# Performance work log

Measured on AMD Instinct MI355X. Metric: run time of the kernel, lower is better.

## Reference

```python
import jax, jax.numpy as jnp
import numpy as np

E = 64      # n_routed_experts
T = 32768   # total routed tokens
K = 1024    # hidden_size
I = 512     # moe_intermediate_size
C = 1024


def setup_inputs() -> dict:
    key = jax.random.key(0)
    k1, k2, k3 = jax.random.split(key, 3)
    x = jax.random.normal(k1, (T, K), dtype=jnp.float32)
    # uniform routing: 512 tokens per expert, sums to T
    tokens_per_expert = jnp.full((E,), T // E, dtype=jnp.int32)
    w13 = jax.random.normal(k2, (E, K, 2 * I), dtype=jnp.float32) * 0.02  # fused w1/w3
    w2 = jax.random.normal(k3, (E, I, K), dtype=jnp.float32) * 0.02
    return {"x": x, "tokens_per_expert": tokens_per_expert, "w13": w13, "w2": w2, "decoding": 0}


def reference(x, tokens_per_expert, w13, w2, decoding):
    # Tokens are laid out contiguously by expert (grouped-GEMM convention).
    starts = jnp.cumsum(tokens_per_expert) - tokens_per_expert           # [E]
    eid = jnp.repeat(jnp.arange(E), tokens_per_expert, total_repeat_length=T)  # [T]
    pos = jnp.arange(T) - starts[eid]                                    # slot within expert
    # dispatch to dense [E, C, K] buffer (zero-padded beyond each expert's count)
    xb = jnp.zeros((E, C, K), x.dtype).at[eid, pos].set(x)
    # grouped GEMM 1: fused w1w3  -> [E, C, 2I]
    gate_up = jnp.einsum('eck,ekn->ecn', xb, w13)
    # SwiGLU: split last dim into gate / up
    gate, up = jnp.split(gate_up, 2, axis=-1)
    h = jax.nn.silu(gate) * up                                           # [E, C, I]
    # grouped GEMM 2: fused w2 -> [E, C, K]
    yb = jnp.einsum('eci,eik->eck', h, w2)
    # gather back to token order [T, K]
    return yb[eid, pos]
```

## Files before the change

### kernel.cpp

```cpp
#include <hip/hip_runtime.h>
#include <hip/hip_bf16.h>
#include <stdint.h>

#define NEXP 64
#define TTOK 32768
#define HID  1024
#define IMID 512
#define CAP  1024

typedef __bf16 bf16x8 __attribute__((ext_vector_type(8)));
typedef float  f32x4  __attribute__((ext_vector_type(4)));

static __device__ __forceinline__ unsigned int f2bf_u(float f) {
    __hip_bfloat16 h = __float2bfloat16(f);
    return (unsigned int)*reinterpret_cast<unsigned short*>(&h);
}
static __device__ __forceinline__ unsigned int pack2(float lo, float hi) {
    return f2bf_u(lo) | (f2bf_u(hi) << 16);
}
static __device__ __forceinline__ unsigned short f2bf_s(float f) {
    __hip_bfloat16 h = __float2bfloat16(f);
    return *reinterpret_cast<unsigned short*>(&h);
}

static __device__ __forceinline__ void gload16(const void* g, void* l) {
    __builtin_amdgcn_global_load_lds(
        (const __attribute__((address_space(1))) unsigned int*)g,
        (__attribute__((address_space(3))) unsigned int*)l,
        16, 0, 0);
}

static __device__ __forceinline__ int expert_start(const int* tpe, int e, int lane) {
    int v = tpe[lane];
    int contrib = (lane < e) ? v : 0;
    #pragma unroll
    for (int off = 1; off < 64; off <<= 1)
        contrib += __shfl_xor(contrib, off, 64);
    return contrib;
}

__global__ __launch_bounds__(256)
void cvt_all_k(const float* __restrict__ x, unsigned short* __restrict__ xbf,
               const float* __restrict__ w13, unsigned short* __restrict__ w13p) {
    const int bid = blockIdx.x;
    const int t   = threadIdx.x;

    if (bid < 16384) {
        const int n0 = (bid & 15) * 64;
        const int k0 = ((bid >> 4) & 15) * 64;
        const int e  = bid >> 8;
        __shared__ unsigned short Tl[64][72];
        const int kl = t >> 4, nl = (t & 15) * 4;
        const float* src = w13 + ((size_t)e << 20) + (size_t)k0 * 1024 + n0;
        #pragma unroll
        for (int p = 0; p < 4; ++p) {
            int k = kl + p * 16;
            f32x4 v = *reinterpret_cast<const f32x4*>(src + (size_t)k * 1024 + nl);
            uint2 wv; wv.x = pack2(v.x, v.y); wv.y = pack2(v.z, v.w);
            *reinterpret_cast<uint2*>(&Tl[k][nl]) = wv;
        }
        __syncthreads();
        const int nloc = t >> 2, kc = (t & 3) * 16;
        const int n = n0 + nloc;
        const int icol = n & 511, isup = n >> 9;
        const int np = (icol >> 5) * 64 + isup * 32 + (icol & 31);
        unsigned int v32[8];
        #pragma unroll
        for (int j = 0; j < 8; ++j)
            v32[j] = (unsigned int)Tl[kc + 2 * j][nloc] |
                     ((unsigned int)Tl[kc + 2 * j + 1][nloc] << 16);
        unsigned short* dst = w13p + ((size_t)e << 20) + (size_t)np * 1024 + k0 + kc;
        uint4 o0 = {v32[0], v32[1], v32[2], v32[3]};
        uint4 o1 = {v32[4], v32[5], v32[6], v32[7]};
        *reinterpret_cast<uint4*>(dst)     = o0;
        *reinterpret_cast<uint4*>(dst + 8) = o1;
    } else {
        size_t i = ((size_t)(bid - 16384) * 256 + t) * 8;
        f32x4 a = *reinterpret_cast<const f32x4*>(x + i);
        f32x4 b = *reinterpret_cast<const f32x4*>(x + i + 4);
        uint4 o;
        o.x = pack2(a.x, a.y); o.y = pack2(a.z, a.w);
        o.z = pack2(b.x, b.y); o.w = pack2(b.z, b.w);
        *reinterpret_cast<uint4*>(xbf + i) = o;
    }
}

static __device__ __forceinline__ void w2_tile_cvt(const float* __restrict__ w2,
                                                   unsigned short* __restrict__ w2p,
                                                   int tile, int t, char* lds) {
    const int e  = tile >> 7;
    const int k0 = ((tile >> 4) & 7) * 64;
    const int n0 = (tile & 15) * 64;
    unsigned short (*Tl)[72] = reinterpret_cast<unsigned short(*)[72]>(lds);
    const int kl = t >> 4, nl = (t & 15) * 4;
    const float* src = w2 + (size_t)e * (IMID * HID) + (size_t)k0 * 1024 + n0;
    #pragma unroll
    for (int p = 0; p < 4; ++p) {
        int k = kl + p * 16;
        f32x4 v = *reinterpret_cast<const f32x4*>(src + (size_t)k * 1024 + nl);
        uint2 wv; wv.x = pack2(v.x, v.y); wv.y = pack2(v.z, v.w);
        *reinterpret_cast<uint2*>(&Tl[k][nl]) = wv;
    }
    __syncthreads();
    const int nloc = t >> 2, kc = (t & 3) * 16;
    unsigned int v32[8];
    #pragma unroll
    for (int j = 0; j < 8; ++j)
        v32[j] = (unsigned int)Tl[kc + 2 * j][nloc] |
                 ((unsigned int)Tl[kc + 2 * j + 1][nloc] << 16);
    unsigned short* dst = w2p + (size_t)e * (HID * IMID) + (size_t)(n0 + nloc) * IMID + k0 + kc;
    uint4 o0 = {v32[0], v32[1], v32[2], v32[3]};
    uint4 o1 = {v32[4], v32[5], v32[6], v32[7]};
    *reinterpret_cast<uint4*>(dst)     = o0;
    *reinterpret_cast<uint4*>(dst + 8) = o1;
}

__global__ __launch_bounds__(256, 2)
void gemm1(const unsigned short* __restrict__ xbf,
           const int* __restrict__ tpe,
           const unsigned short* __restrict__ w13p,
           unsigned short* __restrict__ hbuf,
           const float* __restrict__ w2,
           unsigned short* __restrict__ w2p) {
    __shared__ alignas(16) char lds[49152];
    const int bid = blockIdx.x;
    const int t = threadIdx.x, lane = t & 63, w = t >> 6;

    if (bid >= 2048) {
        w2_tile_cvt(w2, w2p, bid - 2048, t, lds);
        return;
    }

    const int work = (bid & 7) * 256 + (bid >> 3);
    const int e  = work >> 5;
    const int nt = (work >> 3) & 3;
    const int mt = work & 7;

    int cnt = tpe[e]; if (cnt > CAP) cnt = CAP;
    const int m0 = mt * 128;
    if (m0 >= cnt) return;
    const int start = expert_start(tpe, e, lane);

    char* As = lds;
    char* Bs = lds + 16384;
    const int wr = w >> 1, wc = w & 1;
    const int r = lane & 15, q = lane >> 4;

    f32x4 acc[4][8];
    const f32x4 z4 = {0.f, 0.f, 0.f, 0.f};
    #pragma unroll
    for (int i = 0; i < 4; ++i)
        #pragma unroll
        for (int j = 0; j < 8; ++j) acc[i][j] = z4;

    const int swb = ((lane & 7) ^ (lane >> 3)) << 4;
    const char* aP = (const char*)xbf;
    const char* bP = (const char*)w13p + ((size_t)e << 21) + ((size_t)nt << 19);

    for (int kt = 0; kt < 16; ++kt) {
        __syncthreads();
        const int kb = kt * 128;
        #pragma unroll
        for (int i = 0; i < 4; ++i) {
            const int srow = w * 32 + i * 8 + (lane >> 3);
            long ar = (long)start + m0 + srow;
            if (ar > TTOK - 1) ar = TTOK - 1;
            gload16(aP + ar * 2048 + kb + swb, As + w * 4096 + i * 1024);
        }
        #pragma unroll
        for (int i = 0; i < 8; ++i) {
            const int srow = w * 64 + i * 8 + (lane >> 3);
            gload16(bP + (size_t)srow * 2048 + kb + swb, Bs + w * 8192 + i * 1024);
        }
        __syncthreads();
        #pragma unroll
        for (int kk = 0; kk < 2; ++kk) {
            bf16x8 af[4], bf[8];
            #pragma unroll
            for (int fm = 0; fm < 4; ++fm) {
                int row = (wr << 6) + (fm << 4) + r;
                af[fm] = *reinterpret_cast<const bf16x8*>(
                    As + row * 128 + ((kk * 64 + q * 16) ^ ((row & 7) << 4)));
            }
            #pragma unroll
            for (int fn = 0; fn < 8; ++fn) {
                int row = (wc << 7) + (fn << 4) + r;
                bf[fn] = *reinterpret_cast<const bf16x8*>(
                    Bs + row * 128 + ((kk * 64 + q * 16) ^ ((row & 7) << 4)));
            }
            #pragma unroll
            for (int fm = 0; fm < 4; ++fm)
                #pragma unroll
                for (int fn = 0; fn < 8; ++fn)
                    acc[fm][fn] = __builtin_amdgcn_mfma_f32_16x16x32_bf16(
                        af[fm], bf[fn], acc[fm][fn], 0, 0, 0);
        }
    }

    #pragma unroll
    for (int fm = 0; fm < 4; ++fm) {
        int mb = m0 + (wr << 6) + (fm << 4) + (q << 2);
        #pragma unroll
        for (int c2 = 0; c2 < 2; ++c2) {
            #pragma unroll
            for (int fp = 0; fp < 2; ++fp) {
                f32x4 g = acc[fm][c2 * 4 + fp];
                f32x4 u = acc[fm][c2 * 4 + 2 + fp];
                int icol = (nt * 4 + wc * 2 + c2) * 32 + fp * 16 + r;
                #pragma unroll
                for (int v = 0; v < 4; ++v) {
                    if (mb + v < cnt) {
                        float gv = g[v];
                        float sv = (gv / (1.f + __expf(-gv))) * u[v];
                        hbuf[(size_t)(start + mb + v) * IMID + icol] = f2bf_s(sv);
                    }
                }
            }
        }
    }
}

__global__ __launch_bounds__(256, 2)
void gemm2(const unsigned short* __restrict__ hbuf,
           const int* __restrict__ tpe,
           const unsigned short* __restrict__ w2p,
           float* __restrict__ out) {
    __shared__ alignas(16) char lds[49152];
    const int bid  = blockIdx.x;
    const int work = (bid & 7) * 256 + (bid >> 3);
    const int e  = work >> 5;
    const int nt = (work >> 3) & 3;
    const int mt = work & 7;

    const int t = threadIdx.x, lane = t & 63, w = t >> 6;
    int cnt = tpe[e]; if (cnt > CAP) cnt = CAP;
    const int m0 = mt * 128;
    if (m0 >= cnt) return;
    const int start = expert_start(tpe, e, lane);

    char* As = lds;
    char* Bs = lds + 16384;
    const int wr = w >> 1, wc = w & 1;
    const int r = lane & 15, q = lane >> 4;

    f32x4 acc[4][8];
    const f32x4 z4 = {0.f, 0.f, 0.f, 0.f};
    #pragma unroll
    for (int i = 0; i < 4; ++i)
        #pragma unroll
        for (int j = 0; j < 8; ++j) acc[i][j] = z4;

    const int swb = ((lane & 7) ^ (lane >> 3)) << 4;
    const char* aP = (const char*)hbuf;
    const char* bP = (const char*)w2p + ((size_t)e << 20) + ((size_t)nt << 18);

    for (int kt = 0; kt < 8; ++kt) {
        __syncthreads();
        const int kb = kt * 128;
        #pragma unroll
        for (int i = 0; i < 4; ++i) {
            const int srow = w * 32 + i * 8 + (lane >> 3);
            long ar = (long)start + m0 + srow;
            if (ar > TTOK - 1) ar = TTOK - 1;
            gload16(aP + ar * 1024 + kb + swb, As + w * 4096 + i * 1024);
        }
        #pragma unroll
        for (int i = 0; i < 8; ++i) {
            const int srow = w * 64 + i * 8 + (lane >> 3);
            gload16(bP + (size_t)srow * 1024 + kb + swb, Bs + w * 8192 + i * 1024);
        }
        __syncthreads();
        #pragma unroll
        for (int kk = 0; kk < 2; ++kk) {
            bf16x8 af[4], bf[8];
            #pragma unroll
            for (int fm = 0; fm < 4; ++fm) {
                int row = (wr << 6) + (fm << 4) + r;
                af[fm] = *reinterpret_cast<const bf16x8*>(
                    As + row * 128 + ((kk * 64 + q * 16) ^ ((row & 7) << 4)));
            }
            #pragma unroll
            for (int fn = 0; fn < 8; ++fn) {
                int row = (wc << 7) + (fn << 4) + r;
                bf[fn] = *reinterpret_cast<const bf16x8*>(
                    Bs + row * 128 + ((kk * 64 + q * 16) ^ ((row & 7) << 4)));
            }
            #pragma unroll
            for (int fm = 0; fm < 4; ++fm)
                #pragma unroll
                for (int fn = 0; fn < 8; ++fn)
                    acc[fm][fn] = __builtin_amdgcn_mfma_f32_16x16x32_bf16(
                        af[fm], bf[fn], acc[fm][fn], 0, 0, 0);
        }
    }

    #pragma unroll
    for (int fm = 0; fm < 4; ++fm) {
        int mb = m0 + (wr << 6) + (fm << 4) + (q << 2);
        #pragma unroll
        for (int fn = 0; fn < 8; ++fn) {
            int ocol = (nt << 8) + (wc << 7) + (fn << 4) + r;
            #pragma unroll
            for (int v = 0; v < 4; ++v) {
                if (mb + v < cnt)
                    out[(size_t)(start + mb + v) * HID + ocol] = acc[fm][fn][v];
            }
        }
    }
}

extern "C" void kernel_launch(void* const* d_in, const int* in_sizes, int n_in,
                              void* d_out, int out_size, void* d_ws, size_t ws_size,
                              hipStream_t stream) {
    const float* x   = (const float*)d_in[0];
    const int*   tpe = (const int*)d_in[1];
    const float* w13 = (const float*)d_in[2];
    const float* w2  = (const float*)d_in[3];
    float* out = (float*)d_out;

    char* ws = (char*)d_ws;
    unsigned short* xbf  = (unsigned short*)(ws);
    unsigned short* hbuf = (unsigned short*)(ws + 67108864);
    unsigned short* w13p = (unsigned short*)(ws + 67108864 + 33554432);
    unsigned short* w2p  = (unsigned short*)(ws + 67108864 + 33554432 + 134217728);

    cvt_all_k<<<dim3(32768, 1, 1), dim3(256, 1, 1), 0, stream>>>(x, xbf, w13, w13p);
    gemm1    <<<dim3(10240, 1, 1), dim3(256, 1, 1), 0, stream>>>(xbf, tpe, w13p, hbuf, w2, w2p);
    gemm2    <<<dim3(2048, 1, 1), dim3(256, 1, 1), 0, stream>>>(hbuf, tpe, w2p, out);
}
```

Baseline: 284.6 us.

## Split w13 conversion across phases to overlap with gemm1 halves

Converts x and only the first half of the experts' w13 weights in the first kernel. The second half of w13 is converted alongside gemm1 for experts 0-31, and the w2 conversion runs alongside gemm1 for experts 32-63. The aim is to hide the memory-bound fp32→bf16 weight conversion behind compute-bound GEMM blocks instead of running it serially up front. This adds one more kernel launch, and the mixed blocks in each grid compete for resources.

```diff
diff --git a/kernel.cpp b/kernel.cpp
--- a/kernel.cpp
+++ b/kernel.cpp
@@ -39,50 +39,35 @@
     return contrib;
 }
 
-__global__ __launch_bounds__(256)
-void cvt_all_k(const float* __restrict__ x, unsigned short* __restrict__ xbf,
-               const float* __restrict__ w13, unsigned short* __restrict__ w13p) {
-    const int bid = blockIdx.x;
-    const int t   = threadIdx.x;
-
-    if (bid < 16384) {
-        const int n0 = (bid & 15) * 64;
-        const int k0 = ((bid >> 4) & 15) * 64;
-        const int e  = bid >> 8;
-        __shared__ unsigned short Tl[64][72];
-        const int kl = t >> 4, nl = (t & 15) * 4;
-        const float* src = w13 + ((size_t)e << 20) + (size_t)k0 * 1024 + n0;
-        #pragma unroll
-        for (int p = 0; p < 4; ++p) {
-            int k = kl + p * 16;
-            f32x4 v = *reinterpret_cast<const f32x4*>(src + (size_t)k * 1024 + nl);
-            uint2 wv; wv.x = pack2(v.x, v.y); wv.y = pack2(v.z, v.w);
-            *reinterpret_cast<uint2*>(&Tl[k][nl]) = wv;
-        }
-        __syncthreads();
-        const int nloc = t >> 2, kc = (t & 3) * 16;
-        const int n = n0 + nloc;
-        const int icol = n & 511, isup = n >> 9;
-        const int np = (icol >> 5) * 64 + isup * 32 + (icol & 31);
-        unsigned int v32[8];
-        #pragma unroll
-        for (int j = 0; j < 8; ++j)
-            v32[j] = (unsigned int)Tl[kc + 2 * j][nloc] |
-                     ((unsigned int)Tl[kc + 2 * j + 1][nloc] << 16);
-        unsigned short* dst = w13p + ((size_t)e << 20) + (size_t)np * 1024 + k0 + kc;
-        uint4 o0 = {v32[0], v32[1], v32[2], v32[3]};
-        uint4 o1 = {v32[4], v32[5], v32[6], v32[7]};
-        *reinterpret_cast<uint4*>(dst)     = o0;
-        *reinterpret_cast<uint4*>(dst + 8) = o1;
-    } else {
-        size_t i = ((size_t)(bid - 16384) * 256 + t) * 8;
-        f32x4 a = *reinterpret_cast<const f32x4*>(x + i);
-        f32x4 b = *reinterpret_cast<const f32x4*>(x + i + 4);
-        uint4 o;
-        o.x = pack2(a.x, a.y); o.y = pack2(a.z, a.w);
-        o.z = pack2(b.x, b.y); o.w = pack2(b.z, b.w);
-        *reinterpret_cast<uint4*>(xbf + i) = o;
-    }
+
+static __device__ __forceinline__ void w13_tile_cvt(const float* __restrict__ w13,
+                                                    unsigned short* __restrict__ w13p,
+                                                    int e, int k0, int n0, int t, char* lds) {
+    unsigned short (*Tl)[72] = reinterpret_cast<unsigned short(*)[72]>(lds);
+    const int kl = t >> 4, nl = (t & 15) * 4;
+    const float* src = w13 + ((size_t)e << 20) + (size_t)k0 * 1024 + n0;
+    #pragma unroll
+    for (int p = 0; p < 4; ++p) {
+        int k = kl + p * 16;
+        f32x4 v = *reinterpret_cast<const f32x4*>(src + (size_t)k * 1024 + nl);
+        uint2 wv; wv.x = pack2(v.x, v.y); wv.y = pack2(v.z, v.w);
+        *reinterpret_cast<uint2*>(&Tl[k][nl]) = wv;
+    }
+    __syncthreads();
+    const int nloc = t >> 2, kc = (t & 3) * 16;
+    const int n = n0 + nloc;
+    const int icol = n & 511, isup = n >> 9;
+    const int np = (icol >> 5) * 64 + isup * 32 + (icol & 31);
+    unsigned int v32[8];
+    #pragma unroll
+    for (int j = 0; j < 8; ++j)
+        v32[j] = (unsigned int)Tl[kc + 2 * j][nloc] |
+                 ((unsigned int)Tl[kc + 2 * j + 1][nloc] << 16);
+    unsigned short* dst = w13p + ((size_t)e << 20) + (size_t)np * 1024 + k0 + kc;
+    uint4 o0 = {v32[0], v32[1], v32[2], v32[3]};
+    uint4 o1 = {v32[4], v32[5], v32[6], v32[7]};
+    *reinterpret_cast<uint4*>(dst)     = o0;
+    *reinterpret_cast<uint4*>(dst + 8) = o1;
 }
 
 static __device__ __forceinline__ void w2_tile_cvt(const float* __restrict__ w2,
@@ -115,26 +100,15 @@
     *reinterpret_cast<uint4*>(dst + 8) = o1;
 }
 
-__global__ __launch_bounds__(256, 2)
-void gemm1(const unsigned short* __restrict__ xbf,
-           const int* __restrict__ tpe,
-           const unsigned short* __restrict__ w13p,
-           unsigned short* __restrict__ hbuf,
-           const float* __restrict__ w2,
-           unsigned short* __restrict__ w2p) {
-    __shared__ alignas(16) char lds[49152];
-    const int bid = blockIdx.x;
-    const int t = threadIdx.x, lane = t & 63, w = t >> 6;
-
-    if (bid >= 2048) {
-        w2_tile_cvt(w2, w2p, bid - 2048, t, lds);
-        return;
-    }
-
-    const int work = (bid & 7) * 256 + (bid >> 3);
-    const int e  = work >> 5;
+static __device__ __forceinline__ void gemm1_body(
+    const unsigned short* __restrict__ xbf, const int* __restrict__ tpe,
+    const unsigned short* __restrict__ w13p, unsigned short* __restrict__ hbuf,
+    int ebase, int bid, int t, char* lds) {
+    const int work = (bid & 7) * 128 + (bid >> 3);
+    const int e  = ebase + (work >> 5);
     const int nt = (work >> 3) & 3;
     const int mt = work & 7;
+    const int lane = t & 63, w = t >> 6;
 
     int cnt = tpe[e]; if (cnt > CAP) cnt = CAP;
     const int m0 = mt * 128;
@@ -220,6 +194,61 @@
     }
 }
 
+__global__ __launch_bounds__(256)
+void phase1(const float* __restrict__ x, unsigned short* __restrict__ xbf,
+            const float* __restrict__ w13, unsigned short* __restrict__ w13p) {
+    __shared__ alignas(16) char lds[9216];
+    const int bid = blockIdx.x;
+    const int t   = threadIdx.x;
+    if (bid < 16384) {
+        size_t i = ((size_t)bid * 256 + t) * 8;
+        f32x4 a = *reinterpret_cast<const f32x4*>(x + i);
+        f32x4 b = *reinterpret_cast<const f32x4*>(x + i + 4);
+        uint4 o;
+        o.x = pack2(a.x, a.y); o.y = pack2(a.z, a.w);
+        o.z = pack2(b.x, b.y); o.w = pack2(b.z, b.w);
+        *reinterpret_cast<uint4*>(xbf + i) = o;
+    } else {
+        const int tile = bid - 16384;
+        const int e  = tile >> 8;
+        const int k0 = ((tile >> 4) & 15) * 64;
+        const int n0 = (tile & 15) * 64;
+        w13_tile_cvt(w13, w13p, e, k0, n0, t, lds);
+    }
+}
+
+__global__ __launch_bounds__(256, 2)
+void phase2(const unsigned short* __restrict__ xbf, const int* __restrict__ tpe,
+            const unsigned short* __restrict__ w13p, unsigned short* __restrict__ hbuf,
+            const float* __restrict__ w13) {
+    __shared__ alignas(16) char lds[49152];
+    const int bid = blockIdx.x;
+    const int t   = threadIdx.x;
+    if (bid < 1024) {
+        gemm1_body(xbf, tpe, w13p, hbuf, 0, bid, t, lds);
+    } else {
+        const int tile = bid - 1024;
+        const int e  = 32 + (tile >> 8);
+        const int k0 = ((tile >> 4) & 15) * 64;
+        const int n0 = (tile & 15) * 64;
+        w13_tile_cvt(w13, (unsigned short*)w13p, e, k0, n0, t, lds);
+    }
+}
+
+__global__ __launch_bounds__(256, 2)
+void phase3(const unsigned short* __restrict__ xbf, const int* __restrict__ tpe,
+            const unsigned short* __restrict__ w13p, unsigned short* __restrict__ hbuf,
+            const float* __restrict__ w2, unsigned short* __restrict__ w2p) {
+    __shared__ alignas(16) char lds[49152];
+    const int bid = blockIdx.x;
+    const int t   = threadIdx.x;
+    if (bid < 1024) {
+        gemm1_body(xbf, tpe, w13p, hbuf, 32, bid, t, lds);
+    } else {
+        w2_tile_cvt(w2, w2p, bid - 1024, t, lds);
+    }
+}
+
 __global__ __launch_bounds__(256, 2)
 void gemm2(const unsigned short* __restrict__ hbuf,
            const int* __restrict__ tpe,
@@ -324,7 +353,8 @@
     unsigned short* w13p = (unsigned short*)(ws + 67108864 + 33554432);
     unsigned short* w2p  = (unsigned short*)(ws + 67108864 + 33554432 + 134217728);
 
-    cvt_all_k<<<dim3(32768, 1, 1), dim3(256, 1, 1), 0, stream>>>(x, xbf, w13, w13p);
-    gemm1    <<<dim3(10240, 1, 1), dim3(256, 1, 1), 0, stream>>>(xbf, tpe, w13p, hbuf, w2, w2p);
-    gemm2    <<<dim3(2048, 1, 1), dim3(256, 1, 1), 0, stream>>>(hbuf, tpe, w2p, out);
-}
+    phase1<<<dim3(24576, 1, 1), dim3(256, 1, 1), 0, stream>>>(x, xbf, w13, w13p);
+    phase2<<<dim3(9216, 1, 1), dim3(256, 1, 1), 0, stream>>>(xbf, tpe, w13p, hbuf, w13);
+    phase3<<<dim3(9216, 1, 1), dim3(256, 1, 1), 0, stream>>>(xbf, tpe, w13p, hbuf, w2, w2p);
+    gemm2 <<<dim3(2048, 1, 1), dim3(256, 1, 1), 0, stream>>>(hbuf, tpe, w2p, out);
+}
```

After: 285.4 us. No clear change (+0.3%).
